# Performance work log

Measured on AMD Instinct MI355X. Metric: run time of the kernel, lower is better.

## Reference

```python
import jax, jax.numpy as jnp
import numpy as np
import math

B, S, D, H, M, R = 4, 1024, 1024, 16, 4, 64
DH = D // H
EPS = 1e-8

def setup_inputs() -> dict:
    key = jax.random.key(0)
    ks = jax.random.split(key, 8)
    sc = 0.02
    return {
        'x': jax.random.normal(ks[0], (B, S, D), jnp.float32),
        'Wk': jax.random.normal(ks[1], (D, D), jnp.float32) * sc,
        'bk': jnp.zeros((D,), jnp.float32),
        'Wq': jax.random.normal(ks[2], (D, D), jnp.float32) * sc,
        'bq': jnp.zeros((D,), jnp.float32),
        'Wv': jax.random.normal(ks[3], (D, D), jnp.float32) * sc,
        'bv': jnp.zeros((D,), jnp.float32),
        'mask1': jax.random.normal(ks[4], (M, R, S), jnp.float32) * sc,
        'mask2': jax.random.normal(ks[5], (M, R, S), jnp.float32) * sc,
        'roll_back': jax.random.randint(ks[6], (M, S, S), 0, S, jnp.int64),
    }

def reference(x, Wk, bk, Wq, bq, Wv, bv, mask1, mask2, roll_back):
    def proj(W, b):
        # torch Linear: x @ W^T + b ; reshape to [B, H, S, DH]
        y = jnp.dot(x, W.T) + b
        return y.reshape(B, S, H, DH).transpose(0, 2, 1, 3)
    k = proj(Wk, bk)
    q = proj(Wq, bq)
    v = proj(Wv, bv)
    # learnable low-rank mask: [M, S, S]
    learnable_mask = jnp.einsum('mrs,mrt->mst', mask1, mask2)
    # gather along last dim with roll_back indices
    gathered = jnp.take_along_axis(learnable_mask, roll_back, axis=-1)  # [M, S, S]
    att = jnp.einsum('bhsd,bhtd->bhst', q, k) / math.sqrt(DH)  # [B, H, S, S]
    att = att.reshape(B, H // M, M, S, S) * gathered[None, None]
    att = att.reshape(B, H, S, S)
    # Frobenius norm over last two dims per (B, H)
    fro = jnp.sqrt(jnp.sum(att * att, axis=(-2, -1), keepdims=True))
    att = att / (fro + EPS)
    out = jnp.einsum('bhst,bhtd->bhsd', att, v)
    return out.transpose(0, 2, 1, 3).reshape(B, S, D)
```

## Files before the change

kernel.cpp:

```cpp
#include <hip/hip_runtime.h>
#include <hip/hip_bf16.h>
#include <stdint.h>

typedef __attribute__((ext_vector_type(8))) __bf16 bf16x8;
typedef __attribute__((ext_vector_type(4))) float  f32x4;

__device__ __forceinline__ ushort f2bf(float f) {
    union { float f; uint32_t u; } v; v.f = f;
    uint32_t u = v.u;
    uint32_t r = 0x7FFFu + ((u >> 16) & 1u);
    return (ushort)((u + r) >> 16);
}
__device__ __forceinline__ float bf2f(ushort u) {
    union { uint32_t u; float f; } v; v.u = ((uint32_t)u) << 16;
    return v.f;
}
__device__ __forceinline__ uint32_t pack2bf(float a, float b) {
    return (uint32_t)f2bf(a) | ((uint32_t)f2bf(b) << 16);
}

typedef __attribute__((address_space(3))) uint32_t lds_u32_t;
typedef const __attribute__((address_space(1))) uint32_t glb_u32_t;
__device__ __forceinline__ void async_copy16(const void* g, void* l) {
    __builtin_amdgcn_global_load_lds((glb_u32_t*)g, (lds_u32_t*)l, 16, 0, 0);
}

__global__ __launch_bounds__(256) void prep(
    const float* __restrict__ x, const float* __restrict__ wk,
    const float* __restrict__ wq, const float* __restrict__ wv,
    const float* __restrict__ m1, const float* __restrict__ m2,
    const int* __restrict__ rb,
    ushort* __restrict__ xb, ushort* __restrict__ wball, ushort* __restrict__ gth)
{
    __shared__ float As8[64 * 8];
    __shared__ float lmS[8 * 1024];
    const int tid = threadIdx.x;
    if (blockIdx.x >= 512) {
        int i = (blockIdx.x - 512) * 256 + tid;
        const float* src; ushort* dst; int j;
        if (i < 1048576) { src = x; dst = xb; j = i; }
        else {
            int t = i - 1048576;
            int z = t >> 18;
            j = t & 262143;
            src = (z == 0) ? wk : (z == 1) ? wq : wv;
            dst = wball + z * 1048576;
        }
        float4 f = ((const float4*)src)[j];
        ushort4 o;
        o.x = f2bf(f.x); o.y = f2bf(f.y); o.z = f2bf(f.z); o.w = f2bf(f.w);
        ((ushort4*)dst)[j] = o;
        return;
    }
    const int s0 = (blockIdx.x & 127) * 8;
    const int m = blockIdx.x >> 7;
    if (tid < 128) {
        int r = tid >> 1, half = tid & 1;
        *(float4*)&As8[r * 8 + half * 4] =
            *(const float4*)&m1[(m * 64 + r) * 1024 + s0 + half * 4];
    }
    __syncthreads();
    f32x4 acc8[8];
    #pragma unroll
    for (int s = 0; s < 8; s++) acc8[s] = (f32x4){0.f, 0.f, 0.f, 0.f};
    const float* m2b = m2 + m * 65536 + tid * 4;
    #pragma unroll 4
    for (int r = 0; r < 64; r++) {
        float4 b4 = *(const float4*)&m2b[r * 1024];
        f32x4 b = (f32x4){b4.x, b4.y, b4.z, b4.w};
        #pragma unroll
        for (int s = 0; s < 8; s++) acc8[s] += As8[r * 8 + s] * b;
    }
    #pragma unroll
    for (int s = 0; s < 8; s++)
        *(f32x4*)&lmS[s * 1024 + tid * 4] = acc8[s];
    __syncthreads();
    const int base = (m * 1024 + s0) * 1024;
    #pragma unroll
    for (int i = 0; i < 8; i++) {
        int c = tid + i * 256;
        int row = c >> 8, j = (c & 255) * 4;
        int4 idx = *(const int4*)&rb[base + row * 1024 + j];
        ushort4 o;
        o.x = f2bf(lmS[row * 1024 + (idx.x & 1023)] * 0.125f);
        o.y = f2bf(lmS[row * 1024 + (idx.y & 1023)] * 0.125f);
        o.z = f2bf(lmS[row * 1024 + (idx.z & 1023)] * 0.125f);
        o.w = f2bf(lmS[row * 1024 + (idx.w & 1023)] * 0.125f);
        *(ushort4*)&gth[base + row * 1024 + j] = o;
    }
}

__global__ __launch_bounds__(256, 2) void proj_gemm(
    const ushort* __restrict__ xb, const ushort* __restrict__ wball,
    const float* __restrict__ bk, const float* __restrict__ bq, const float* __restrict__ bv,
    ushort* __restrict__ kd, ushort* __restrict__ qd, ushort* __restrict__ vd)
{
    __shared__ ushort As[2][128 * 64];
    __shared__ ushort Bs[2][128 * 64];
    const int g = blockIdx.x;
    const int col0 = (g & 7) * 128;
    const int t = g >> 3;
    const int row0 = (t & 31) * 128;
    const int z = t >> 5;
    const ushort* wb = wball + z * 1048576;
    const int tid = threadIdx.x;
    const int lane = tid & 63, wave = tid >> 6;
    const int quad = lane >> 4, m15 = lane & 15;
    const int wr = wave >> 1, wc = wave & 1;

    f32x4 acc[4][4];
    for (int i = 0; i < 4; i++)
        for (int j = 0; j < 4; j++) acc[i][j] = (f32x4){0.f, 0.f, 0.f, 0.f};

    auto stage = [&](int buf, int kk) {
        #pragma unroll
        for (int i = 0; i < 4; i++) {
            int c = tid + i * 256;
            int r = c >> 3, cjp = c & 7;
            int cj = cjp ^ (r & 7);
            async_copy16(&xb[(row0 + r) * 1024 + kk + cj * 8], &As[buf][c * 8]);
            async_copy16(&wb[(col0 + r) * 1024 + kk + cj * 8], &Bs[buf][c * 8]);
        }
    };

    stage(0, 0);
    for (int it = 0; it < 16; it++) {
        __syncthreads();
        if (it < 15) stage((it + 1) & 1, (it + 1) * 64);
        const ushort* Ab = As[it & 1];
        const ushort* Bb = Bs[it & 1];
        #pragma unroll
        for (int kh = 0; kh < 2; kh++) {
            bf16x8 af[4], bfv[4];
            #pragma unroll
            for (int fr = 0; fr < 4; fr++) {
                int row = wr * 64 + fr * 16 + m15;
                int q4 = kh * 4 + quad;
                af[fr] = *(const bf16x8*)&Ab[row * 64 + ((q4 ^ (row & 7)) * 8)];
            }
            #pragma unroll
            for (int fc = 0; fc < 4; fc++) {
                int row = wc * 64 + fc * 16 + m15;
                int q4 = kh * 4 + quad;
                bfv[fc] = *(const bf16x8*)&Bs[it & 1][row * 64 + ((q4 ^ (row & 7)) * 8)];
            }
            #pragma unroll
            for (int fr = 0; fr < 4; fr++)
                #pragma unroll
                for (int fc = 0; fc < 4; fc++)
                    acc[fr][fc] = __builtin_amdgcn_mfma_f32_16x16x32_bf16(af[fr], bfv[fc], acc[fr][fc], 0, 0, 0);
        }
    }

    const float* bias = (z == 0) ? bk : (z == 1) ? bq : bv;
    ushort* dstA = (z == 0) ? kd : qd;
    for (int fr = 0; fr < 4; fr++) {
        int ibase = row0 + wr * 64 + fr * 16 + quad * 4;
        int b_ = ibase >> 10, s = ibase & 1023;
        for (int fc = 0; fc < 4; fc++) {
            int j = col0 + wc * 64 + fc * 16 + m15;
            int h = j >> 6, dh = j & 63;
            float bb = bias[j];
            if (z < 2) {
                for (int r = 0; r < 4; r++)
                    dstA[((b_ * 16 + h) * 1024 + (s + r)) * 64 + dh] = f2bf(acc[fr][fc][r] + bb);
            } else {
                ushort4 o;
                o.x = f2bf(acc[fr][fc][0] + bb);
                o.y = f2bf(acc[fr][fc][1] + bb);
                o.z = f2bf(acc[fr][fc][2] + bb);
                o.w = f2bf(acc[fr][fc][3] + bb);
                *(ushort4*)&vd[((b_ * 16 + h) * 64 + dh) * 1024 + s] = o;
            }
        }
    }
}

__global__ __launch_bounds__(256, 2) void attention(
    const ushort* __restrict__ qd, const ushort* __restrict__ kd, const ushort* __restrict__ vd,
    const ushort* __restrict__ gth, float* __restrict__ O, float* __restrict__ ss)
{
    __shared__ ushort Ks[2][64 * 64];
    __shared__ ushort Vs[2][64 * 64];
    __shared__ ushort Ms[2][64 * 64];
    __shared__ ushort Ps[64 * 72];
    __shared__ float Osc[64 * 68];
    __shared__ float red[4];
    const int g = blockIdx.x;
    const int idx = g >> 3;
    const int s0 = (idx & 15) * 64;
    const int bh = (g & 7) + 8 * (idx >> 4);
    const int mm = bh & 3;
    const int tid = threadIdx.x, lane = tid & 63, wave = tid >> 6;
    const int quad = lane >> 4, m15 = lane & 15;
    const int sw = wave * 16 + m15;
    const int sw7 = m15 & 7;
    const ushort* gbase = gth + mm * 1048576 + s0 * 1024;

    #pragma unroll
    for (int i = 0; i < 2; i++) {
        int c = tid + i * 256;
        int r = c >> 3, cj = (c & 7) ^ (r & 7);
        async_copy16(&qd[(bh * 1024 + s0 + r) * 64 + cj * 8], &Ks[0][c * 8]);
    }
    __syncthreads();
    bf16x8 qf[2];
    #pragma unroll
    for (int kk = 0; kk < 2; kk++)
        qf[kk] = *(const bf16x8*)&Ks[0][sw * 64 + (((kk * 4 + quad) ^ sw7) * 8)];
    __syncthreads();

    f32x4 oacc[4];
    #pragma unroll
    for (int i = 0; i < 4; i++) oacc[i] = (f32x4){0.f, 0.f, 0.f, 0.f};
    float ssacc = 0.f;

    auto stage = [&](int buf, int t0) {
        #pragma unroll
        for (int i = 0; i < 2; i++) {
            int c = tid + i * 256;
            int r = c >> 3, cj = (c & 7) ^ (r & 7);
            async_copy16(&kd[(bh * 1024 + t0 + r) * 64 + cj * 8], &Ks[buf][c * 8]);
            async_copy16(&vd[(bh * 64 + r) * 1024 + t0 + cj * 8], &Vs[buf][c * 8]);
            async_copy16(&gbase[r * 1024 + t0 + cj * 8],          &Ms[buf][c * 8]);
        }
    };

    stage(0, 0);
    for (int it = 0; it < 16; it++) {
        __syncthreads();
        if (it < 15) stage((it + 1) & 1, (it + 1) * 64);
        const ushort* Kb = Ks[it & 1];
        const ushort* Vb = Vs[it & 1];
        const ushort* Mb = Ms[it & 1];

        f32x4 pacc[4];
        #pragma unroll
        for (int tc = 0; tc < 4; tc++) {
            f32x4 p = (f32x4){0.f, 0.f, 0.f, 0.f};
            #pragma unroll
            for (int kk = 0; kk < 2; kk++) {
                int row = tc * 16 + m15;
                bf16x8 a = *(const bf16x8*)&Kb[row * 64 + (((kk * 4 + quad) ^ (row & 7)) * 8)];
                p = __builtin_amdgcn_mfma_f32_16x16x32_bf16(a, qf[kk], p, 0, 0, 0);
            }
            pacc[tc] = p;
        }
        #pragma unroll
        for (int tc = 0; tc < 4; tc++) {
            int ch = (tc * 2 + (quad >> 1)) ^ sw7;
            ushort4 mv4 = *(const ushort4*)&Mb[sw * 64 + ch * 8 + (quad & 1) * 4];
            float p0 = pacc[tc][0] * bf2f(mv4.x);
            float p1 = pacc[tc][1] * bf2f(mv4.y);
            float p2 = pacc[tc][2] * bf2f(mv4.z);
            float p3 = pacc[tc][3] * bf2f(mv4.w);
            ssacc += p0 * p0 + p1 * p1 + p2 * p2 + p3 * p3;
            uint2 pw;
            pw.x = pack2bf(p0, p1);
            pw.y = pack2bf(p2, p3);
            *(uint2*)&Ps[sw * 72 + tc * 16 + quad * 4] = pw;
        }
        bf16x8 pf[2];
        #pragma unroll
        for (int kk = 0; kk < 2; kk++)
            pf[kk] = *(const bf16x8*)&Ps[sw * 72 + kk * 32 + quad * 8];
        #pragma unroll
        for (int nc = 0; nc < 4; nc++) {
            #pragma unroll
            for (int kk = 0; kk < 2; kk++) {
                int row = nc * 16 + m15;
                bf16x8 a = *(const bf16x8*)&Vb[row * 64 + (((kk * 4 + quad) ^ (row & 7)) * 8)];
                oacc[nc] = __builtin_amdgcn_mfma_f32_16x16x32_bf16(a, pf[kk], oacc[nc], 0, 0, 0);
            }
        }
    }
    __syncthreads();
    #pragma unroll
    for (int nc = 0; nc < 4; nc++)
        *(f32x4*)&Osc[sw * 68 + nc * 16 + quad * 4] = oacc[nc];
    __syncthreads();
    #pragma unroll
    for (int i = 0; i < 4; i++) {
        int c = tid + i * 256;
        int row = c >> 4, col = (c & 15) * 4;
        f32x4 v4 = *(const f32x4*)&Osc[row * 68 + col];
        *(f32x4*)&O[(bh * 1024 + s0 + row) * 64 + col] = v4;
    }
    for (int off = 32; off; off >>= 1) ssacc += __shfl_down(ssacc, off, 64);
    if (lane == 0) red[wave] = ssacc;
    __syncthreads();
    if (tid == 0) atomicAdd(&ss[bh], red[0] + red[1] + red[2] + red[3]);
}

__global__ __launch_bounds__(256) void normalize_out(const float* __restrict__ O,
                                                     const float* __restrict__ ss,
                                                     float* __restrict__ out)
{
    int gid = blockIdx.x * 256 + threadIdx.x;
    int e = gid * 4;
    int bh = e >> 16;
    float inv = 1.f / (sqrtf(ss[bh]) + 1e-8f);
    float4 v4 = *(const float4*)&O[e];
    int b_ = bh >> 4, h = bh & 15;
    int s = (e >> 6) & 1023, dh = e & 63;
    float4 o4 = {v4.x * inv, v4.y * inv, v4.z * inv, v4.w * inv};
    *(float4*)&out[((b_ * 1024 + s) * 16 + h) * 64 + dh] = o4;
}

extern "C" void kernel_launch(void* const* d_in, const int* in_sizes, int n_in,
                              void* d_out, int out_size, void* d_ws, size_t ws_size,
                              hipStream_t stream) {
    const float* x  = (const float*)d_in[0];
    const float* Wk = (const float*)d_in[1];
    const float* bk = (const float*)d_in[2];
    const float* Wq = (const float*)d_in[3];
    const float* bq = (const float*)d_in[4];
    const float* Wv = (const float*)d_in[5];
    const float* bv = (const float*)d_in[6];
    const float* m1 = (const float*)d_in[7];
    const float* m2 = (const float*)d_in[8];
    const int*   rb = (const int*)d_in[9];
    float* out = (float*)d_out;

    char* ws = (char*)d_ws;
    ushort* xb    = (ushort*)(ws);
    ushort* wball = (ushort*)(ws + 8388608);
    ushort* kd    = (ushort*)(ws + 14680064);
    ushort* qd    = (ushort*)(ws + 23068672);
    ushort* vd    = (ushort*)(ws + 31457280);
    float*  O     = (float*)(ws + 39845888);
    ushort* gth   = (ushort*)(ws + 56623104);
    float*  ssb   = (float*)(ws + 65011712);

    prep<<<7680, 256, 0, stream>>>(x, Wk, Wq, Wv, m1, m2, rb, xb, wball, gth);
    proj_gemm<<<768, 256, 0, stream>>>(xb, wball, bk, bq, bv, kd, qd, vd);
    hipMemsetAsync(ssb, 0, 64 * sizeof(float), stream);
    attention<<<1024, 256, 0, stream>>>(qd, kd, vd, gth, O, ssb);
    normalize_out<<<4096, 256, 0, stream>>>(O, ssb, out);
}
```

Baseline: 206.8 us.

## Load gathered mask directly to registers, shrink LDS, raise attention occupancy

The attention kernel no longer stages the gathered mask tile through LDS. Each lane reads its four mask values straight from global memory into registers. The output staging buffer is halved and written in two passes, and launch bounds go from 2 to 3 blocks per SM, all to cut LDS usage and fit more blocks. The ss buffer is now zeroed inside prep instead of by a separate memset, which removes one API call. The trade-off is that the direct global mask loads are not async and may expose latency, and each thread's row-strided accesses coalesce less well.

```diff
diff --git a/kernel.cpp b/kernel.cpp
--- a/kernel.cpp
+++ b/kernel.cpp
@@ -30,11 +30,13 @@
     const float* __restrict__ wq, const float* __restrict__ wv,
     const float* __restrict__ m1, const float* __restrict__ m2,
     const int* __restrict__ rb,
-    ushort* __restrict__ xb, ushort* __restrict__ wball, ushort* __restrict__ gth)
+    ushort* __restrict__ xb, ushort* __restrict__ wball, ushort* __restrict__ gth,
+    float* __restrict__ ssb)
 {
     __shared__ float As8[64 * 8];
     __shared__ float lmS[8 * 1024];
     const int tid = threadIdx.x;
+    if (blockIdx.x == 0 && tid < 64) ssb[tid] = 0.f;
     if (blockIdx.x >= 512) {
         int i = (blockIdx.x - 512) * 256 + tid;
         const float* src; ushort* dst; int j;
@@ -142,7 +144,7 @@
             for (int fc = 0; fc < 4; fc++) {
                 int row = wc * 64 + fc * 16 + m15;
                 int q4 = kh * 4 + quad;
-                bfv[fc] = *(const bf16x8*)&Bs[it & 1][row * 64 + ((q4 ^ (row & 7)) * 8)];
+                bfv[fc] = *(const bf16x8*)&Bb[row * 64 + ((q4 ^ (row & 7)) * 8)];
             }
             #pragma unroll
             for (int fr = 0; fr < 4; fr++)
@@ -176,15 +178,14 @@
     }
 }
 
-__global__ __launch_bounds__(256, 2) void attention(
+__global__ __launch_bounds__(256, 3) void attention(
     const ushort* __restrict__ qd, const ushort* __restrict__ kd, const ushort* __restrict__ vd,
     const ushort* __restrict__ gth, float* __restrict__ O, float* __restrict__ ss)
 {
     __shared__ ushort Ks[2][64 * 64];
     __shared__ ushort Vs[2][64 * 64];
-    __shared__ ushort Ms[2][64 * 64];
     __shared__ ushort Ps[64 * 72];
-    __shared__ float Osc[64 * 68];
+    __shared__ float Osc[32 * 68];
     __shared__ float red[4];
     const int g = blockIdx.x;
     const int idx = g >> 3;
@@ -195,7 +196,7 @@
     const int quad = lane >> 4, m15 = lane & 15;
     const int sw = wave * 16 + m15;
     const int sw7 = m15 & 7;
-    const ushort* gbase = gth + mm * 1048576 + s0 * 1024;
+    const ushort* mrow = gth + mm * 1048576 + (s0 + sw) * 1024;
 
     #pragma unroll
     for (int i = 0; i < 2; i++) {
@@ -222,17 +223,21 @@
             int r = c >> 3, cj = (c & 7) ^ (r & 7);
             async_copy16(&kd[(bh * 1024 + t0 + r) * 64 + cj * 8], &Ks[buf][c * 8]);
             async_copy16(&vd[(bh * 64 + r) * 1024 + t0 + cj * 8], &Vs[buf][c * 8]);
-            async_copy16(&gbase[r * 1024 + t0 + cj * 8],          &Ms[buf][c * 8]);
         }
     };
 
     stage(0, 0);
     for (int it = 0; it < 16; it++) {
+        const int t0 = it * 64;
         __syncthreads();
-        if (it < 15) stage((it + 1) & 1, (it + 1) * 64);
+        if (it < 15) stage((it + 1) & 1, t0 + 64);
         const ushort* Kb = Ks[it & 1];
         const ushort* Vb = Vs[it & 1];
-        const ushort* Mb = Ms[it & 1];
+
+        ushort4 mv[4];
+        #pragma unroll
+        for (int tc = 0; tc < 4; tc++)
+            mv[tc] = *(const ushort4*)&mrow[t0 + tc * 16 + quad * 4];
 
         f32x4 pacc[4];
         #pragma unroll
@@ -248,12 +253,10 @@
         }
         #pragma unroll
         for (int tc = 0; tc < 4; tc++) {
-            int ch = (tc * 2 + (quad >> 1)) ^ sw7;
-            ushort4 mv4 = *(const ushort4*)&Mb[sw * 64 + ch * 8 + (quad & 1) * 4];
-            float p0 = pacc[tc][0] * bf2f(mv4.x);
-            float p1 = pacc[tc][1] * bf2f(mv4.y);
-            float p2 = pacc[tc][2] * bf2f(mv4.z);
-            float p3 = pacc[tc][3] * bf2f(mv4.w);
+            float p0 = pacc[tc][0] * bf2f(mv[tc].x);
+            float p1 = pacc[tc][1] * bf2f(mv[tc].y);
+            float p2 = pacc[tc][2] * bf2f(mv[tc].z);
+            float p3 = pacc[tc][3] * bf2f(mv[tc].w);
             ssacc += p0 * p0 + p1 * p1 + p2 * p2 + p3 * p3;
             uint2 pw;
             pw.x = pack2bf(p0, p1);
@@ -274,17 +277,23 @@
             }
         }
     }
-    __syncthreads();
-    #pragma unroll
-    for (int nc = 0; nc < 4; nc++)
-        *(f32x4*)&Osc[sw * 68 + nc * 16 + quad * 4] = oacc[nc];
-    __syncthreads();
-    #pragma unroll
-    for (int i = 0; i < 4; i++) {
-        int c = tid + i * 256;
-        int row = c >> 4, col = (c & 15) * 4;
-        f32x4 v4 = *(const f32x4*)&Osc[row * 68 + col];
-        *(f32x4*)&O[(bh * 1024 + s0 + row) * 64 + col] = v4;
+    #pragma unroll
+    for (int half = 0; half < 2; half++) {
+        __syncthreads();
+        if ((wave >> 1) == half) {
+            int row = (wave & 1) * 16 + m15;
+            #pragma unroll
+            for (int nc = 0; nc < 4; nc++)
+                *(f32x4*)&Osc[row * 68 + nc * 16 + quad * 4] = oacc[nc];
+        }
+        __syncthreads();
+        #pragma unroll
+        for (int i = 0; i < 2; i++) {
+            int c = tid + i * 256;
+            int row = c >> 4, col = (c & 15) * 4;
+            f32x4 v4 = *(const f32x4*)&Osc[row * 68 + col];
+            *(f32x4*)&O[(bh * 1024 + s0 + half * 32 + row) * 64 + col] = v4;
+        }
     }
     for (int off = 32; off; off >>= 1) ssacc += __shfl_down(ssacc, off, 64);
     if (lane == 0) red[wave] = ssacc;
@@ -332,9 +341,8 @@
     ushort* gth   = (ushort*)(ws + 56623104);
     float*  ssb   = (float*)(ws + 65011712);
 
-    prep<<<7680, 256, 0, stream>>>(x, Wk, Wq, Wv, m1, m2, rb, xb, wball, gth);
+    prep<<<7680, 256, 0, stream>>>(x, Wk, Wq, Wv, m1, m2, rb, xb, wball, gth, ssb);
     proj_gemm<<<768, 256, 0, stream>>>(xb, wball, bk, bq, bv, kd, qd, vd);
-    hipMemsetAsync(ssb, 0, 64 * sizeof(float), stream);
     attention<<<1024, 256, 0, stream>>>(qd, kd, vd, gth, O, ssb);
     normalize_out<<<4096, 256, 0, stream>>>(O, ssb, out);
 }
```

New measurement: 234.0 us. +13.2%, slower.
